# Optimization experiments

Hardware: AMD Instinct MI355X
Metric: run time of the kernel (lower is better)

Reference implementation:

```python
import jax, jax.numpy as jnp
import numpy as np

B, S, D, H, F = 4, 1024, 2048, 16, 8192
HD = D // H  # head dim = 128
EPS = 1e-5


def layer_norm(x, w, b):
    mu = jnp.mean(x, axis=-1, keepdims=True)
    var = jnp.mean(jnp.square(x - mu), axis=-1, keepdims=True)
    return (x - mu) * jax.lax.rsqrt(var + EPS) * w + b


def setup_inputs() -> dict:
    key = jax.random.key(0)
    ks = jax.random.split(key, 12)
    s = 0.02  # realistic init scale for weights
    return {
        "x": jax.random.normal(ks[0], (B, S, D), jnp.float32),
        "attention_mask": jnp.zeros((B, 1, 1, S), jnp.float32),
        "wq": jax.random.normal(ks[1], (D, D), jnp.float32) * s,
        "bq": jax.random.normal(ks[2], (D,), jnp.float32) * s,
        "wk": jax.random.normal(ks[3], (D, D), jnp.float32) * s,
        "bk": jax.random.normal(ks[4], (D,), jnp.float32) * s,
        "wv": jax.random.normal(ks[5], (D, D), jnp.float32) * s,
        "bv": jax.random.normal(ks[6], (D,), jnp.float32) * s,
        "wo": jax.random.normal(ks[7], (D, D), jnp.float32) * s,
        "bo": jax.random.normal(ks[8], (D,), jnp.float32) * s,
        "ln1_w": jnp.ones((D,), jnp.float32),
        "ln1_b": jnp.zeros((D,), jnp.float32),
        "wi": jax.random.normal(ks[9], (F, D), jnp.float32) * s,
        "bi": jax.random.normal(ks[10], (F,), jnp.float32) * s,
        "wo2": jax.random.normal(ks[11], (D, F), jnp.float32) * s,
        "bo2": jnp.zeros((D,), jnp.float32),
        "ln2_w": jnp.ones((D,), jnp.float32),
        "ln2_b": jnp.zeros((D,), jnp.float32),
    }


def reference(x, attention_mask, wq, bq, wk, bk, wv, bv, wo, bo,
              ln1_w, ln1_b, wi, bi, wo2, bo2, ln2_w, ln2_b):
    # --- self attention ---
    q = (jnp.einsum('bsd,ed->bse', x, wq) + bq).reshape(B, S, H, HD).transpose(0, 2, 1, 3)
    k = (jnp.einsum('bsd,ed->bse', x, wk) + bk).reshape(B, S, H, HD).transpose(0, 2, 1, 3)
    v = (jnp.einsum('bsd,ed->bse', x, wv) + bv).reshape(B, S, H, HD).transpose(0, 2, 1, 3)
    scores = jnp.einsum('bhqd,bhkd->bhqk', q, k) / jnp.sqrt(jnp.float32(HD))
    scores = scores + attention_mask  # additive mask, broadcast over heads/query
    probs = jax.nn.softmax(scores, axis=-1)
    ctx = jnp.einsum('bhqk,bhkd->bhqd', probs, v)
    ctx = ctx.transpose(0, 2, 1, 3).reshape(B, S, D)
    # --- attention output: dense + bias + residual + LayerNorm ---
    attn_out = layer_norm(jnp.einsum('bsd,ed->bse', ctx, wo) + bo + x, ln1_w, ln1_b)
    # --- FFN: intermediate dense + bias, GELU, output dense + bias + residual + LN ---
    inter = jnp.einsum('bsd,fd->bsf', attn_out, wi) + bi
    h = jax.nn.gelu(inter, approximate=False)
    out = layer_norm(jnp.einsum('bsf,df->bsd', h, wo2) + bo2 + attn_out, ln2_w, ln2_b)
    return out
```

## Files before the change

kernel.cpp:

```cpp
#include <hip/hip_runtime.h>
#include <hip/hip_bf16.h>
#include <cstdint>
#include <cstddef>

typedef __attribute__((ext_vector_type(8))) short short8;
typedef __attribute__((ext_vector_type(4))) float f32x4;

#define DEV static __device__ __forceinline__

constexpr int kS = 1024, kD = 2048, kH = 16, kHD = 128, kF = 8192;
constexpr int kM = 4096;
constexpr float kEPS = 1e-5f;

constexpr size_t SZ_DD   = (size_t)kD * kD * 2;
constexpr size_t SZ_FD   = (size_t)kF * kD * 2;
constexpr size_t SZ_MD16 = (size_t)kM * kD * 2;
constexpr size_t SZ_MD32 = (size_t)kM * kD * 4;
constexpr size_t OFF_WQ  = 0;
constexpr size_t OFF_WK  = OFF_WQ + SZ_DD;
constexpr size_t OFF_WV  = OFF_WK + SZ_DD;
constexpr size_t OFF_WO  = OFF_WV + SZ_DD;
constexpr size_t OFF_WI  = OFF_WO + SZ_DD;
constexpr size_t OFF_WO2 = OFF_WI + SZ_FD;
constexpr size_t OFF_XB  = OFF_WO2 + SZ_FD;
constexpr size_t OFF_Q   = OFF_XB + SZ_MD16;
constexpr size_t OFF_K   = OFF_Q + SZ_MD16;
constexpr size_t OFF_V   = OFF_K + SZ_MD16;
constexpr size_t OFF_H   = OFF_XB;
constexpr size_t OFF_CTX = OFF_V + SZ_MD16;
constexpr size_t OFF_Y1  = OFF_CTX + SZ_MD16;
constexpr size_t OFF_A1B = OFF_Y1 + SZ_MD32;
constexpr size_t OFF_Y2  = OFF_A1B + SZ_MD16;
constexpr size_t WS_NEED = OFF_Y2 + SZ_MD32;

DEV void gload16(const void* g, void* l) {
  __builtin_amdgcn_global_load_lds(
      (const __attribute__((address_space(1))) unsigned int*)g,
      (__attribute__((address_space(3))) unsigned int*)l, 16, 0, 0);
}

__global__ void cvt_bf16(const float* __restrict__ in, __hip_bfloat16* __restrict__ out, int n4) {
  int stride = gridDim.x * blockDim.x;
  for (int i = blockIdx.x * blockDim.x + threadIdx.x; i < n4; i += stride) {
    float4 v = reinterpret_cast<const float4*>(in)[i];
    union { ushort4 u; __hip_bfloat16 h[4]; } o;
    o.h[0] = __float2bfloat16(v.x);
    o.h[1] = __float2bfloat16(v.y);
    o.h[2] = __float2bfloat16(v.z);
    o.h[3] = __float2bfloat16(v.w);
    reinterpret_cast<ushort4*>(out)[i] = o.u;
  }
}

template <int MODE>
__global__ __launch_bounds__(512, 2)
void gemm256(const __hip_bfloat16* __restrict__ A,
             const __hip_bfloat16* __restrict__ Bt,
             const float* __restrict__ bias,
             float* __restrict__ out0, float* __restrict__ out1,
             void* __restrict__ outb,
             int M, int N, int K, int kLen) {
  __shared__ __align__(16) char lds[131072];
  const int tid = threadIdx.x;
  const int lane = tid & 63, w = tid >> 6;
  const int wm = w >> 2, wn = w & 3;
  const int lg = lane >> 4, lr = lane & 15;
  const int gy = M >> 8, gx = N >> 8;
  const int nwg = gridDim.x, orig = blockIdx.x;
  const int l = (orig & 7) * (nwg >> 3) + (orig >> 3);
  const int tilesPer = gx * gy;
  const int spl = l / tilesPer;
  const int rem = l - spl * tilesPer;
  const int bx = rem / gy, by = rem - bx * gy;
  const int m0 = by * 256, n0 = bx * 256;
  const int k0 = spl * kLen;
  const int NT = kLen >> 6;

  const char* gs[8];
  #pragma unroll
  for (int h = 0; h < 4; ++h) {
    const __hip_bfloat16* src = (h < 2) ? A : Bt;
    const int r0 = ((h < 2) ? m0 : n0) + (h & 1) * 128;
    #pragma unroll
    for (int i = 0; i < 2; ++i) {
      int c = i * 512 + tid;
      int row = c >> 3, slot = c & 7;
      gs[h * 2 + i] =
          (const char*)(src + (size_t)(r0 + row) * K + k0 + (slot ^ (row & 7)) * 8);
    }
  }

#define STAGE(P, H, TOFF)                                                          \
  {                                                                                \
    char* dstb = lds + (((H) < 2) ? 0 : 65536) + (P) * 32768 + ((H) & 1) * 16384;  \
    gload16(gs[(H) * 2 + 0] + (TOFF) * 128, dstb + (0 * 512 + tid) * 16);          \
    gload16(gs[(H) * 2 + 1] + (TOFF) * 128, dstb + (1 * 512 + tid) * 16);          \
  }

  auto ldA = [&](int P, int qm, int mr, int kk) {
    int row = qm * 128 + wm * 64 + mr * 16 + lr;
    return *reinterpret_cast<const short8*>(
        lds + P * 32768 + row * 128 + (((kk * 4 + lg) ^ (row & 7)) * 16));
  };
  auto ldB = [&](int P, int qn, int nr, int kk) {
    int row = qn * 128 + wn * 32 + nr * 16 + lr;
    return *reinterpret_cast<const short8*>(
        lds + 65536 + P * 32768 + row * 128 + (((kk * 4 + lg) ^ (row & 7)) * 16));
  };

  f32x4 acc[4][4][2] = {};

#define MFMA_HALF(q, kk, B)                                                     \
  _Pragma("unroll")                                                             \
  for (int mi = 0; mi < 4; ++mi)                                                \
    _Pragma("unroll")                                                           \
    for (int ni = 0; ni < 2; ++ni)                                              \
      acc[q][mi][ni] = __builtin_amdgcn_mfma_f32_16x16x32_bf16(                 \
          av[kk][mi], B[kk][ni], acc[q][mi][ni], 0, 0, 0);

#define WAIT_LGKM(n)                                                            \
  asm volatile("s_waitcnt lgkmcnt(" #n ")" ::: "memory");                       \
  __builtin_amdgcn_sched_barrier(0);

#define TILE_BODY(P, PF)                                                        \
  {                                                                             \
    \
    \
    asm volatile("s_waitcnt vmcnt(0)" ::: "memory");                            \
    __builtin_amdgcn_s_barrier();                                               \
                           \
    _Pragma("unroll")                                                           \
    for (int i = 0; i < 4; ++i) av[0][i] = ldA(P, 0, i, 0);                     \
    _Pragma("unroll")                                                           \
    for (int i = 0; i < 2; ++i) b0[0][i] = ldB(P, 0, i, 0);                     \
    _Pragma("unroll")                                                           \
    for (int i = 0; i < 4; ++i) av[1][i] = ldA(P, 0, i, 1);                     \
    _Pragma("unroll")                                                           \
    for (int i = 0; i < 2; ++i) b0[1][i] = ldB(P, 0, i, 1);                     \
    if (PF) { STAGE((P) ^ 1, 0, 1 + (P)) STAGE((P) ^ 1, 2, 1 + (P)) }           \
    WAIT_LGKM(6)                                                                \
    __builtin_amdgcn_s_setprio(1);                                              \
    MFMA_HALF(0, 0, b0)                                                         \
    WAIT_LGKM(0)                                                                \
    MFMA_HALF(0, 1, b0)                                                         \
    __builtin_amdgcn_s_setprio(0);                                              \
                        \
    _Pragma("unroll")                                                           \
    for (int i = 0; i < 2; ++i) b1[0][i] = ldB(P, 1, i, 0);                     \
    _Pragma("unroll")                                                           \
    for (int i = 0; i < 2; ++i) b1[1][i] = ldB(P, 1, i, 1);                     \
    if (PF) { STAGE((P) ^ 1, 3, 1 + (P)) STAGE((P) ^ 1, 1, 1 + (P)) }           \
    WAIT_LGKM(2)                                                                \
    __builtin_amdgcn_s_setprio(1);                                              \
    MFMA_HALF(1, 0, b1)                                                         \
    WAIT_LGKM(0)                                                                \
    MFMA_HALF(1, 1, b1)                                                         \
    __builtin_amdgcn_s_setprio(0);                                              \
                                           \
    _Pragma("unroll")                                                           \
    for (int i = 0; i < 4; ++i) av[0][i] = ldA(P, 1, i, 0);                     \
    _Pragma("unroll")                                                           \
    for (int i = 0; i < 4; ++i) av[1][i] = ldA(P, 1, i, 1);                     \
    WAIT_LGKM(4)                                                                \
    __builtin_amdgcn_s_setprio(1);                                              \
    MFMA_HALF(2, 0, b1)                                                         \
    WAIT_LGKM(0)                                                                \
    MFMA_HALF(2, 1, b1)                                                         \
    __builtin_amdgcn_s_setprio(0);                                              \
                                        \
    _Pragma("unroll")                                                           \
    for (int i = 0; i < 2; ++i) b0[0][i] = ldB(P, 0, i, 0);                     \
    _Pragma("unroll")                                                           \
    for (int i = 0; i < 2; ++i) b0[1][i] = ldB(P, 0, i, 1);                     \
    WAIT_LGKM(2)                                                                \
    __builtin_amdgcn_s_setprio(1);                                              \
    MFMA_HALF(3, 0, b0)                                                         \
    WAIT_LGKM(0)                                                                \
    MFMA_HALF(3, 1, b0)                                                         \
    __builtin_amdgcn_s_setprio(0);                                              \
  }

  STAGE(0, 0, 0) STAGE(0, 2, 0) STAGE(0, 3, 0) STAGE(0, 1, 0)

  for (int t2 = 0; t2 < NT; t2 += 2) {
    short8 av[2][4], b0[2][2], b1[2][2];
    TILE_BODY(0, true)
    TILE_BODY(1, (t2 + 2 < NT))
    #pragma unroll
    for (int j = 0; j < 8; ++j) gs[j] += 256;
  }
#undef TILE_BODY
#undef MFMA_HALF
#undef WAIT_LGKM
#undef STAGE

  #pragma unroll
  for (int q = 0; q < 4; ++q) {
    const int qm = (q >= 2) ? 1 : 0;
    const int qn = (q == 1 || q == 2) ? 1 : 0;
    #pragma unroll
    for (int ni = 0; ni < 2; ++ni) {
      int col = n0 + qn * 128 + wn * 32 + ni * 16 + lr;
      float bvv = 0.f;
      if constexpr (MODE != 3) bvv = bias[col];
      #pragma unroll
      for (int mi = 0; mi < 4; ++mi) {
        int row0 = m0 + qm * 128 + wm * 64 + mi * 16 + lg * 4;
        #pragma unroll
        for (int r = 0; r < 4; ++r) {
          int row = row0 + r;
          float val = acc[q][mi][ni][r] + bvv;
          if constexpr (MODE == 0) {
            int which = col >> 11;
            int d = col & 2047;
            int hh = d >> 7, hd = d & 127;
            int bb = row >> 10, ss = row & 1023;
            __hip_bfloat16* base = (__hip_bfloat16*)outb + (size_t)which * ((size_t)kM * kD);
            if (which < 2)
              base[(((size_t)(bb * kH + hh)) * kS + ss) * kHD + hd] = __float2bfloat16(val);
            else
              base[(((size_t)(bb * kH + hh)) * kHD + hd) * kS + ss] = __float2bfloat16(val);
          } else if constexpr (MODE == 2) {
            float g = 0.5f * val * (1.0f + erff(val * 0.70710678118654752f));
            ((__hip_bfloat16*)outb)[(size_t)row * N + col] = __float2bfloat16(g);
          } else {
            float* o = spl ? out1 : out0;
            o[(size_t)row * N + col] = val;
          }
        }
      }
    }
  }
}

__global__ __launch_bounds__(512, 4)
void attn_fwd(const __hip_bfloat16* __restrict__ q,
              const __hip_bfloat16* __restrict__ k,
              const __hip_bfloat16* __restrict__ vt,
              const float* __restrict__ mask,
              __hip_bfloat16* __restrict__ ctx) {
  __shared__ __align__(16) char Ks[2][64 * 256];
  __shared__ __align__(16) char Vt[2][128 * 128];
  __shared__ __align__(16) char Ps[8][2048];
  const int tid = threadIdx.x, lane = tid & 63, w = tid >> 6;
  const int lg = lane >> 4, lr = lane & 15;
  const int orig = blockIdx.x;
  const int l = (orig & 7) * 64 + (orig >> 3);
  const int qt = l & 7, bh = l >> 3;
  const int b = bh >> 4;

  short8 qf[4];
  {
    const __hip_bfloat16* qp =
        q + ((size_t)bh * kS + qt * 128 + w * 16 + lr) * kHD + lg * 8;
    #pragma unroll
    for (int kk = 0; kk < 4; ++kk) qf[kk] = *reinterpret_cast<const short8*>(qp + kk * 32);
  }

  auto stage = [&](int bufi, int t) {
    #pragma unroll
    for (int i = 0; i < 2; ++i) {
      int c = i * 512 + tid;
      int row = c >> 4, slot = c & 15;
      gload16(k + ((size_t)bh * kS + t * 64 + row) * kHD + (slot ^ (row & 15)) * 8,
              Ks[bufi] + c * 16);
    }
    #pragma unroll
    for (int i = 0; i < 2; ++i) {
      int c = i * 512 + tid;
      int row = c >> 3, slot = c & 7;
      gload16(vt + ((size_t)bh * kHD + row) * kS + t * 64 + (slot ^ (row & 7)) * 8,
              Vt[bufi] + c * 16);
    }
  };

  f32x4 o[8] = {};
  float mrun[4], lrun[4];
  #pragma unroll
  for (int r = 0; r < 4; ++r) { mrun[r] = -1e30f; lrun[r] = 0.f; }
  const float scale = 0.08838834764831845f;

  stage(0, 0);
  __syncthreads();

  int buf = 0;
  for (int t = 0; t < 16; ++t) {
    if (t + 1 < 16) stage(buf ^ 1, t + 1);

    f32x4 sacc[4] = {};
    #pragma unroll
    for (int j = 0; j < 4; ++j) {
      int key = j * 16 + lr;
      #pragma unroll
      for (int kk = 0; kk < 4; ++kk) {
        short8 bfrag = *reinterpret_cast<const short8*>(
            Ks[buf] + key * 256 + (((kk * 4 + lg) ^ (key & 15)) * 16));
        sacc[j] = __builtin_amdgcn_mfma_f32_16x16x32_bf16(qf[kk], bfrag, sacc[j], 0, 0, 0);
      }
    }
    float sarr[4][4];
    #pragma unroll
    for (int j = 0; j < 4; ++j) {
      float mv = mask[(size_t)b * kS + t * 64 + j * 16 + lr];
      #pragma unroll
      for (int r = 0; r < 4; ++r) sarr[j][r] = sacc[j][r] * scale + mv;
    }
    #pragma unroll
    for (int r = 0; r < 4; ++r) {
      float tm = fmaxf(fmaxf(sarr[0][r], sarr[1][r]), fmaxf(sarr[2][r], sarr[3][r]));
      #pragma unroll
      for (int d = 1; d < 16; d <<= 1) tm = fmaxf(tm, __shfl_xor(tm, d));
      float mnew = fmaxf(mrun[r], tm);
      float alpha = __expf(mrun[r] - mnew);
      mrun[r] = mnew;
      float rs = 0.f;
      #pragma unroll
      for (int j = 0; j < 4; ++j) {
        float p = __expf(sarr[j][r] - mnew);
        sarr[j][r] = p;
        rs += p;
      }
      #pragma unroll
      for (int d = 1; d < 16; d <<= 1) rs += __shfl_xor(rs, d);
      lrun[r] = lrun[r] * alpha + rs;
      #pragma unroll
      for (int n = 0; n < 8; ++n) o[n][r] *= alpha;
    }
    #pragma unroll
    for (int r = 0; r < 4; ++r) {
      int qr = lg * 4 + r;
      #pragma unroll
      for (int j = 0; j < 4; ++j)
        *reinterpret_cast<__hip_bfloat16*>(
            Ps[w] + ((qr * 128 + (j * 16 + lr) * 2) ^ ((qr & 7) << 4))) =
            __float2bfloat16(sarr[j][r]);
    }
    #pragma unroll
    for (int kk2 = 0; kk2 < 2; ++kk2) {
      short8 pa = *reinterpret_cast<const short8*>(
          Ps[w] + ((lr * 128 + kk2 * 64 + lg * 16) ^ ((lr & 7) << 4)));
      #pragma unroll
      for (int n = 0; n < 8; ++n) {
        int hd = n * 16 + lr;
        short8 vb = *reinterpret_cast<const short8*>(
            Vt[buf] + hd * 128 + (((kk2 * 4 + lg) ^ (hd & 7)) * 16));
        o[n] = __builtin_amdgcn_mfma_f32_16x16x32_bf16(pa, vb, o[n], 0, 0, 0);
      }
    }
    __syncthreads();
    buf ^= 1;
  }

  const int h = bh & 15;
  #pragma unroll
  for (int r = 0; r < 4; ++r) {
    float inv = 1.0f / lrun[r];
    int srow = qt * 128 + w * 16 + lg * 4 + r;
    __hip_bfloat16* cp = ctx + ((size_t)b * kS + srow) * kD + h * 128 + lr;
    #pragma unroll
    for (int n = 0; n < 8; ++n) cp[n * 16] = __float2bfloat16(o[n][r] * inv);
  }
}

template <bool WB16>
__global__ void ln_fuse(const float* __restrict__ p0, const float* __restrict__ p1,
                        const float* __restrict__ bias, const float* __restrict__ res,
                        const float* __restrict__ w, const float* __restrict__ b,
                        float* __restrict__ outf, __hip_bfloat16* __restrict__ outb) {
  const int row = blockIdx.x, tid = threadIdx.x;
  const size_t base = (size_t)row * kD;
  float v[8];
  #pragma unroll
  for (int i = 0; i < 2; ++i) {
    int c4 = tid * 2 + i;
    float4 a  = reinterpret_cast<const float4*>(p0 + base)[c4];
    float4 bb = reinterpret_cast<const float4*>(p1 + base)[c4];
    float4 rr = reinterpret_cast<const float4*>(res + base)[c4];
    float4 bs = reinterpret_cast<const float4*>(bias)[c4];
    v[i * 4 + 0] = a.x + bb.x + rr.x + bs.x;
    v[i * 4 + 1] = a.y + bb.y + rr.y + bs.y;
    v[i * 4 + 2] = a.z + bb.z + rr.z + bs.z;
    v[i * 4 + 3] = a.w + bb.w + rr.w + bs.w;
  }
  float s = 0.f;
  #pragma unroll
  for (int i = 0; i < 8; ++i) s += v[i];
  #pragma unroll
  for (int off = 32; off > 0; off >>= 1) s += __shfl_down(s, off);
  __shared__ float r1[4], r2[4];
  if ((tid & 63) == 0) r1[tid >> 6] = s;
  __syncthreads();
  float mean = (r1[0] + r1[1] + r1[2] + r1[3]) * (1.0f / kD);
  float qv = 0.f;
  #pragma unroll
  for (int i = 0; i < 8; ++i) { float d = v[i] - mean; qv += d * d; }
  #pragma unroll
  for (int off = 32; off > 0; off >>= 1) qv += __shfl_down(qv, off);
  if ((tid & 63) == 0) r2[tid >> 6] = qv;
  __syncthreads();
  float rstd = rsqrtf((r2[0] + r2[1] + r2[2] + r2[3]) * (1.0f / kD) + kEPS);
  #pragma unroll
  for (int i = 0; i < 8; ++i) {
    int col = tid * 8 + i;
    float ov = (v[i] - mean) * rstd * w[col] + b[col];
    outf[base + col] = ov;
    if constexpr (WB16) outb[base + col] = __float2bfloat16(ov);
  }
}

extern "C" void kernel_launch(void* const* d_in, const int* in_sizes, int n_in,
                              void* d_out, int out_size, void* d_ws, size_t ws_size,
                              hipStream_t stream) {
  (void)in_sizes; (void)n_in; (void)out_size;
  if (ws_size < WS_NEED) return;
  const float* x    = (const float*)d_in[0];
  const float* mask = (const float*)d_in[1];
  const float* wq   = (const float*)d_in[2];
  const float* bq   = (const float*)d_in[3];
  const float* wk   = (const float*)d_in[4];
  const float* bk   = (const float*)d_in[5];
  const float* wv   = (const float*)d_in[6];
  const float* bv   = (const float*)d_in[7];
  const float* wo   = (const float*)d_in[8];
  const float* bo   = (const float*)d_in[9];
  const float* l1w  = (const float*)d_in[10];
  const float* l1b  = (const float*)d_in[11];
  const float* wi   = (const float*)d_in[12];
  const float* bi   = (const float*)d_in[13];
  const float* wo2  = (const float*)d_in[14];
  const float* bo2  = (const float*)d_in[15];
  const float* l2w  = (const float*)d_in[16];
  const float* l2b  = (const float*)d_in[17];

  char* ws = (char*)d_ws;
  __hip_bfloat16* wqb  = (__hip_bfloat16*)(ws + OFF_WQ);
  __hip_bfloat16* wkb  = (__hip_bfloat16*)(ws + OFF_WK);
  __hip_bfloat16* wvb  = (__hip_bfloat16*)(ws + OFF_WV);
  __hip_bfloat16* wob  = (__hip_bfloat16*)(ws + OFF_WO);
  __hip_bfloat16* wib  = (__hip_bfloat16*)(ws + OFF_WI);
  __hip_bfloat16* wo2b = (__hip_bfloat16*)(ws + OFF_WO2);
  __hip_bfloat16* xb   = (__hip_bfloat16*)(ws + OFF_XB);
  __hip_bfloat16* qb   = (__hip_bfloat16*)(ws + OFF_Q);
  __hip_bfloat16* kb2  = (__hip_bfloat16*)(ws + OFF_K);
  __hip_bfloat16* vtb  = (__hip_bfloat16*)(ws + OFF_V);
  __hip_bfloat16* hb   = (__hip_bfloat16*)(ws + OFF_H);
  __hip_bfloat16* ctxb = (__hip_bfloat16*)(ws + OFF_CTX);
  __hip_bfloat16* a1b  = (__hip_bfloat16*)(ws + OFF_A1B);
  float* y1   = (float*)(ws + OFF_Y1);
  float* y2   = (float*)(ws + OFF_Y2);
  float* f2p  = (float*)(ws + OFF_WQ);
  float* bqkv = (float*)(ws + OFF_Y2);

  cvt_bf16<<<2048, 256, 0, stream>>>(x,   xb,   kM * kD / 4);
  cvt_bf16<<<1024, 256, 0, stream>>>(wq,  wqb,  kD * kD / 4);
  cvt_bf16<<<1024, 256, 0, stream>>>(wk,  wkb,  kD * kD / 4);
  cvt_bf16<<<1024, 256, 0, stream>>>(wv,  wvb,  kD * kD / 4);
  cvt_bf16<<<1024, 256, 0, stream>>>(wo,  wob,  kD * kD / 4);
  cvt_bf16<<<2048, 256, 0, stream>>>(wi,  wib,  kF * kD / 4);
  cvt_bf16<<<2048, 256, 0, stream>>>(wo2, wo2b, kF * kD / 4);
  hipMemcpyAsync(bqkv,          bq, kD * 4, hipMemcpyDeviceToDevice, stream);
  hipMemcpyAsync(bqkv + kD,     bk, kD * 4, hipMemcpyDeviceToDevice, stream);
  hipMemcpyAsync(bqkv + 2 * kD, bv, kD * 4, hipMemcpyDeviceToDevice, stream);

  dim3 blk(512);
  gemm256<0><<<dim3(384), blk, 0, stream>>>(
      xb, wqb, bqkv, nullptr, nullptr, qb, kM, 6144, kD, kD);
  attn_fwd<<<dim3(512), dim3(512), 0, stream>>>(qb, kb2, vtb, mask, ctxb);
  gemm256<3><<<dim3(256), blk, 0, stream>>>(
      ctxb, wob, nullptr, y1, y2, nullptr, kM, kD, kD, kD / 2);
  ln_fuse<true><<<kM, 256, 0, stream>>>(y1, y2, bo, x, l1w, l1b, y1, a1b);
  gemm256<2><<<dim3(512), blk, 0, stream>>>(
      a1b, wib, bi, nullptr, nullptr, hb, kM, kF, kD, kD);
  gemm256<3><<<dim3(256), blk, 0, stream>>>(
      hb, wo2b, nullptr, y2, f2p, nullptr, kM, kD, kF, kF / 2);
  ln_fuse<false><<<kM, 256, 0, stream>>>(y2, f2p, bo2, y1, l2w, l2b, (float*)d_out, nullptr);
}
```

Baseline: 667.7 us.

## Store V row-major from QKV GEMM and transpose into LDS inside attention

The QKV projection epilogue now writes V in the same [b,h,s,hd] layout as Q and K instead of a transposed [b,h,hd,s] layout, so its stores are no longer strided along the sequence axis. The attention kernel loads V tiles into registers with 8-byte global loads, then writes them to LDS as a swizzled transpose after the PV MFMAs, prefetching one tile ahead. This aims to remove the scattered writes in the GEMM epilogue. In exchange it adds register pressure, narrower global loads and a register-to-LDS transpose inside the attention loop.

```diff
diff --git a/kernel.cpp b/kernel.cpp
--- a/kernel.cpp
+++ b/kernel.cpp
@@ -124,8 +124,7 @@
 
 #define TILE_BODY(P, PF)                                                        \
   {                                                                             \
-    \
-    \
+          \
     asm volatile("s_waitcnt vmcnt(0)" ::: "memory");                            \
     __builtin_amdgcn_s_barrier();                                               \
                            \
@@ -216,10 +215,7 @@
             int hh = d >> 7, hd = d & 127;
             int bb = row >> 10, ss = row & 1023;
             __hip_bfloat16* base = (__hip_bfloat16*)outb + (size_t)which * ((size_t)kM * kD);
-            if (which < 2)
-              base[(((size_t)(bb * kH + hh)) * kS + ss) * kHD + hd] = __float2bfloat16(val);
-            else
-              base[(((size_t)(bb * kH + hh)) * kHD + hd) * kS + ss] = __float2bfloat16(val);
+            base[(((size_t)(bb * kH + hh)) * kS + ss) * kHD + hd] = __float2bfloat16(val);
           } else if constexpr (MODE == 2) {
             float g = 0.5f * val * (1.0f + erff(val * 0.70710678118654752f));
             ((__hip_bfloat16*)outb)[(size_t)row * N + col] = __float2bfloat16(g);
@@ -236,7 +232,7 @@
 __global__ __launch_bounds__(512, 4)
 void attn_fwd(const __hip_bfloat16* __restrict__ q,
               const __hip_bfloat16* __restrict__ k,
-              const __hip_bfloat16* __restrict__ vt,
+              const __hip_bfloat16* __restrict__ v,
               const float* __restrict__ mask,
               __hip_bfloat16* __restrict__ ctx) {
   __shared__ __align__(16) char Ks[2][64 * 256];
@@ -248,6 +244,7 @@
   const int l = (orig & 7) * 64 + (orig >> 3);
   const int qt = l & 7, bh = l >> 3;
   const int b = bh >> 4;
+  const int s4 = tid >> 5, hd4 = tid & 31;
 
   short8 qf[4];
   {
@@ -257,7 +254,7 @@
     for (int kk = 0; kk < 4; ++kk) qf[kk] = *reinterpret_cast<const short8*>(qp + kk * 32);
   }
 
-  auto stage = [&](int bufi, int t) {
+  auto stageK = [&](int bufi, int t) {
     #pragma unroll
     for (int i = 0; i < 2; ++i) {
       int c = i * 512 + tid;
@@ -265,12 +262,23 @@
       gload16(k + ((size_t)bh * kS + t * 64 + row) * kHD + (slot ^ (row & 15)) * 8,
               Ks[bufi] + c * 16);
     }
-    #pragma unroll
-    for (int i = 0; i < 2; ++i) {
-      int c = i * 512 + tid;
-      int row = c >> 3, slot = c & 7;
-      gload16(vt + ((size_t)bh * kHD + row) * kS + t * 64 + (slot ^ (row & 7)) * 8,
-              Vt[bufi] + c * 16);
+  };
+  union VU { uint2 u; ushort s[4]; };
+  VU vr[4];
+  auto loadV = [&](int t) {
+    #pragma unroll
+    for (int i = 0; i < 4; ++i)
+      vr[i].u = *reinterpret_cast<const uint2*>(
+          v + ((size_t)bh * kS + t * 64 + s4 * 4 + i) * kHD + hd4 * 4);
+  };
+  auto writeV = [&](int bufi) {
+    #pragma unroll
+    for (int j = 0; j < 4; ++j) {
+      int hd = hd4 * 4 + j;
+      ushort4 o;
+      o.x = vr[0].s[j]; o.y = vr[1].s[j]; o.z = vr[2].s[j]; o.w = vr[3].s[j];
+      *reinterpret_cast<ushort4*>(
+          Vt[bufi] + hd * 128 + (((s4 >> 1) ^ (hd & 7)) << 4) + ((s4 & 1) << 3)) = o;
     }
   };
 
@@ -280,12 +288,14 @@
   for (int r = 0; r < 4; ++r) { mrun[r] = -1e30f; lrun[r] = 0.f; }
   const float scale = 0.08838834764831845f;
 
-  stage(0, 0);
+  stageK(0, 0);
+  loadV(0);
+  writeV(0);
   __syncthreads();
 
   int buf = 0;
   for (int t = 0; t < 16; ++t) {
-    if (t + 1 < 16) stage(buf ^ 1, t + 1);
+    if (t + 1 < 16) { stageK(buf ^ 1, t + 1); loadV(t + 1); }
 
     f32x4 sacc[4] = {};
     #pragma unroll
@@ -347,6 +357,7 @@
         o[n] = __builtin_amdgcn_mfma_f32_16x16x32_bf16(pa, vb, o[n], 0, 0, 0);
       }
     }
+    if (t + 1 < 16) writeV(buf ^ 1);
     __syncthreads();
     buf ^= 1;
   }
@@ -442,7 +453,7 @@
   __hip_bfloat16* xb   = (__hip_bfloat16*)(ws + OFF_XB);
   __hip_bfloat16* qb   = (__hip_bfloat16*)(ws + OFF_Q);
   __hip_bfloat16* kb2  = (__hip_bfloat16*)(ws + OFF_K);
-  __hip_bfloat16* vtb  = (__hip_bfloat16*)(ws + OFF_V);
+  __hip_bfloat16* vb2  = (__hip_bfloat16*)(ws + OFF_V);
   __hip_bfloat16* hb   = (__hip_bfloat16*)(ws + OFF_H);
   __hip_bfloat16* ctxb = (__hip_bfloat16*)(ws + OFF_CTX);
   __hip_bfloat16* a1b  = (__hip_bfloat16*)(ws + OFF_A1B);
@@ -465,7 +476,7 @@
   dim3 blk(512);
   gemm256<0><<<dim3(384), blk, 0, stream>>>(
       xb, wqb, bqkv, nullptr, nullptr, qb, kM, 6144, kD, kD);
-  attn_fwd<<<dim3(512), dim3(512), 0, stream>>>(qb, kb2, vtb, mask, ctxb);
+  attn_fwd<<<dim3(512), dim3(512), 0, stream>>>(qb, kb2, vb2, mask, ctxb);
   gemm256<3><<<dim3(256), blk, 0, stream>>>(
       ctxb, wob, nullptr, y1, y2, nullptr, kM, kD, kD, kD / 2);
   ln_fuse<true><<<kM, 256, 0, stream>>>(y1, y2, bo, x, l1w, l1b, y1, a1b);
```

Measured after the change: 673.8 us. About the same (+0.9%).
